# Kernel tuning notes

Hardware: AMD Instinct MI355X
Metric: run time of the kernel (lower is better)

## Reference

```python
import jax, jax.numpy as jnp
import numpy as np

N_NODES = 100000
N_EDGES = 3200000
IN_C, HID_C, OUT_C = 128, 128, 64
NUM_GRAPHS = 1024


def sage_conv(x, edge_index, W_l, b_l, W_r):
    # PyG SAGEConv (aggr='mean', root_weight=True):
    #   out = lin_l(mean_{j in N(i)} x_j) + lin_r(x_i)
    src, dst = edge_index[0], edge_index[1]
    msg = x[src]                                             # [E, C] gather
    summed = jax.ops.segment_sum(msg, dst, num_segments=x.shape[0])
    cnt = jax.ops.segment_sum(jnp.ones((msg.shape[0],), x.dtype), dst,
                              num_segments=x.shape[0])
    mean_nb = summed / jnp.maximum(cnt, 1.0)[:, None]        # [N, C]
    return mean_nb @ W_l + b_l + x @ W_r


def setup_inputs() -> dict:
    key = jax.random.key(0)
    ks = jax.random.split(key, 8)
    x = jax.random.normal(ks[0], (N_NODES, IN_C), dtype=jnp.float32)
    edge_index = jax.random.randint(ks[1], (2, N_EDGES), 0, N_NODES, dtype=jnp.int64)
    batch = jnp.sort(jax.random.randint(ks[2], (N_NODES,), 0, NUM_GRAPHS, dtype=jnp.int64))
    s1 = 1.0 / np.sqrt(IN_C)
    s2 = 1.0 / np.sqrt(HID_C)
    W1_l = jax.random.uniform(ks[3], (IN_C, HID_C), jnp.float32, -s1, s1)
    b1 = jax.random.uniform(ks[4], (HID_C,), jnp.float32, -s1, s1)
    W1_r = jax.random.uniform(ks[5], (IN_C, HID_C), jnp.float32, -s1, s1)
    W2_l = jax.random.uniform(ks[6], (HID_C, OUT_C), jnp.float32, -s2, s2)
    b2 = jnp.zeros((OUT_C,), jnp.float32)
    W2_r = jax.random.uniform(ks[7], (HID_C, OUT_C), jnp.float32, -s2, s2)
    return {"x": x, "W1_l": W1_l, "b1": b1, "W1_r": W1_r,
            "W2_l": W2_l, "b2": b2, "W2_r": W2_r,
            "edge_index": edge_index, "batch": batch}


def reference(x, W1_l, b1, W1_r, W2_l, b2, W2_r, edge_index, batch):
    h = sage_conv(x, edge_index, W1_l, b1, W1_r)
    h = jax.nn.relu(h)
    # dropout is identity in eval mode (training=False)
    h = sage_conv(h, edge_index, W2_l, b2, W2_r)
    # global_mean_pool: segment mean over graph ids
    summed = jax.ops.segment_sum(h, batch, num_segments=NUM_GRAPHS)
    cnt = jax.ops.segment_sum(jnp.ones((h.shape[0],), h.dtype), batch,
                              num_segments=NUM_GRAPHS)
    return summed / jnp.maximum(cnt, 1.0)[:, None]           # [NUM_GRAPHS, OUT_C]
```

## Files before the change

kernel.cpp:

```cpp
#include <hip/hip_runtime.h>


constexpr int NN = 100000;
constexpr int NE = 3200000;
constexpr int C1 = 128;
constexpr int C2 = 64;
constexpr int NG = 1024;

constexpr int NBK = (NN + 511) >> 9;
constexpr int CAP = 18176;
constexpr int NSH = 13;

typedef unsigned int u32;
typedef unsigned short u16;
typedef unsigned char u8;
typedef _Float16 f16;
typedef f16 f16x8 __attribute__((ext_vector_type(8)));
typedef float f32x4 __attribute__((ext_vector_type(4)));

__device__ __forceinline__ float h2f(u32 bits16) {
  f16 h; u16 b = (u16)bits16;
  __builtin_memcpy(&h, &b, 2);
  return (float)h;
}
__device__ __forceinline__ u16 f2h(float f) {
  f16 h = (f16)f; u16 b;
  __builtin_memcpy(&b, &h, 2);
  return b;
}
__device__ __forceinline__ u32 packh2(float a, float b) {
  return (u32)f2h(a) | ((u32)f2h(b) << 16);
}
__device__ __forceinline__ u32 packq4(float a, float b, float c, float d) {
  int q = 0;
  q = __builtin_amdgcn_cvt_pk_fp8_f32(a, b, q, false);
  q = __builtin_amdgcn_cvt_pk_fp8_f32(c, d, q, true);
  return (u32)q;
}
__device__ __forceinline__ void acc4(u32 g, float& a0, float& a1,
                                     float& a2, float& a3) {
  const auto p = __builtin_amdgcn_cvt_pk_f32_fp8((int)g, false);
  const auto q = __builtin_amdgcn_cvt_pk_f32_fp8((int)g, true);
  a0 += p[0]; a1 += p[1]; a2 += q[0]; a3 += q[1];
}
__device__ __forceinline__ uint4 q8toh8(uint2 g) {
  const auto p0 = __builtin_amdgcn_cvt_pk_f32_fp8((int)g.x, false);
  const auto p1 = __builtin_amdgcn_cvt_pk_f32_fp8((int)g.x, true);
  const auto p2 = __builtin_amdgcn_cvt_pk_f32_fp8((int)g.y, false);
  const auto p3 = __builtin_amdgcn_cvt_pk_f32_fp8((int)g.y, true);
  uint4 o;
  o.x = packh2(p0[0], p0[1]);
  o.y = packh2(p1[0], p1[1]);
  o.z = packh2(p2[0], p2[1]);
  o.w = packh2(p3[0], p3[1]);
  return o;
}

__global__ __launch_bounds__(256)
void sage_x2hw(const float* __restrict__ x, u16* __restrict__ xh,
               u32* __restrict__ xq,
               const float* __restrict__ W1l, const float* __restrict__ W1r,
               const float* __restrict__ W2l, const float* __restrict__ W2r,
               u16* __restrict__ wt1, u16* __restrict__ wt2,
               int* __restrict__ gcur) {
  const int id = blockIdx.x * 256 + threadIdx.x;
  constexpr int NX = NN * 32;
  if (id < NX) {
    const float4 v = ((const float4*)x)[id];
    uint2 o;
    o.x = packh2(v.x, v.y);
    o.y = packh2(v.z, v.w);
    ((uint2*)xh)[id] = o;
    xq[id] = packq4(v.x, v.y, v.z, v.w);
  } else if (id < NX + 128 * 256) {
    const int id2 = id - NX;
    const int n = id2 >> 8, k = id2 & 255;
    const float v = (k < 128) ? W1l[k * 128 + n] : W1r[(k - 128) * 128 + n];
    wt1[id2] = f2h(v);
  } else if (id < NX + 128 * 256 + 128 * 128) {
    const int id3 = id - NX - 128 * 256;
    const int n = id3 >> 7, k = id3 & 127;
    const float v = (n < 64) ? W2l[k * 64 + n] : W2r[k * 64 + (n - 64)];
    wt2[id3] = f2h(v);
  } else if (id < NX + 128 * 256 + 128 * 128 + NBK) {
    const int b = id - NX - 128 * 256 - 128 * 128;
    gcur[b] = b * CAP;
  }
}

__global__ __launch_bounds__(256)
void sage_part(const int* __restrict__ esrc, const int* __restrict__ edst,
               int* __restrict__ gcur, u32* __restrict__ gpart) {
  __shared__ int h[NBK], cur[NBK];
  for (int i = threadIdx.x; i < NBK; i += 256) h[i] = 0;
  __syncthreads();
  const int e0 = blockIdx.x * 4096 + threadIdx.x * 4;
  int4 dv[4], sv[4];
  bool val[4];
#pragma unroll
  for (int j = 0; j < 4; ++j) {
    const int e = e0 + j * 1024;
    val[j] = (e < NE);
    if (val[j]) {
      dv[j] = *(const int4*)(edst + e);
      sv[j] = *(const int4*)(esrc + e);
    }
  }
#pragma unroll
  for (int j = 0; j < 4; ++j) {
    if (val[j]) {
      atomicAdd(&h[dv[j].x >> 9], 1);
      atomicAdd(&h[dv[j].y >> 9], 1);
      atomicAdd(&h[dv[j].z >> 9], 1);
      atomicAdd(&h[dv[j].w >> 9], 1);
    }
  }
  __syncthreads();
  for (int i = threadIdx.x; i < NBK; i += 256)
    cur[i] = h[i] ? atomicAdd(&gcur[i], h[i]) : 0;
  __syncthreads();
#pragma unroll
  for (int j = 0; j < 4; ++j) {
    if (val[j]) {
      int bk, p;
      bk = dv[j].x >> 9; p = atomicAdd(&cur[bk], 1);
      if (p < (bk + 1) * CAP) gpart[p] = ((u32)sv[j].x << 9) | (u32)(dv[j].x & 511);
      bk = dv[j].y >> 9; p = atomicAdd(&cur[bk], 1);
      if (p < (bk + 1) * CAP) gpart[p] = ((u32)sv[j].y << 9) | (u32)(dv[j].y & 511);
      bk = dv[j].z >> 9; p = atomicAdd(&cur[bk], 1);
      if (p < (bk + 1) * CAP) gpart[p] = ((u32)sv[j].z << 9) | (u32)(dv[j].z & 511);
      bk = dv[j].w >> 9; p = atomicAdd(&cur[bk], 1);
      if (p < (bk + 1) * CAP) gpart[p] = ((u32)sv[j].w << 9) | (u32)(dv[j].w & 511);
    }
  }
}

__global__ __launch_bounds__(256)
void sage_pscan(const int* __restrict__ gcur, int* __restrict__ bbase) {
  __shared__ int s[256];
  const int t = threadIdx.x;
  int c = (t < NBK) ? (gcur[t] - t * CAP) : 0;
  c = (c > CAP) ? CAP : c;
  s[t] = c;
  __syncthreads();
  for (int d = 1; d < 256; d <<= 1) {
    const int a = (t >= d) ? s[t - d] : 0;
    __syncthreads();
    s[t] += a;
    __syncthreads();
  }
  if (t < NBK) bbase[t] = s[t] - c;
  if (t == 255) bbase[NBK] = s[255];
}

__global__ __launch_bounds__(512)
void sage_bbuild(const int* __restrict__ bbase, const u32* __restrict__ gpart,
                 int* __restrict__ offs, int* __restrict__ csr) {
  __shared__ int cnt2[512 * NSH];
  __shared__ int ssc[512];
  const int b = blockIdx.x, t = threadIdx.x;
  const int c0 = bbase[b], cnt = bbase[b + 1] - c0;
  const u32* gp = gpart + (size_t)b * CAP;
  for (int i = t; i < 512 * NSH; i += 512) cnt2[i] = 0;
  __syncthreads();
  for (int e = t; e < cnt; e += 512) {
    const u32 pk = gp[e];
    atomicAdd(&cnt2[(pk & 511) * NSH + (pk >> 22)], 1);
  }
  __syncthreads();
  int deg = 0;
#pragma unroll
  for (int s = 0; s < NSH; ++s) deg += cnt2[t * NSH + s];
  ssc[t] = deg;
  __syncthreads();
  for (int d = 1; d < 512; d <<= 1) {
    const int a = (t >= d) ? ssc[t - d] : 0;
    __syncthreads();
    ssc[t] += a;
    __syncthreads();
  }
  const int pre = ssc[t] - deg;
  const int node = b * 512 + t;
  if (node < NN) offs[node] = c0 + pre;
  if (b == 0 && t == 0) offs[NN] = bbase[NBK];
  int run = c0 + pre;
#pragma unroll
  for (int s = 0; s < NSH; ++s) {
    const int c = cnt2[t * NSH + s];
    cnt2[t * NSH + s] = run;
    run += c;
  }
  __syncthreads();
  for (int e = t; e < cnt; e += 512) {
    const u32 pk = gp[e];
    const int p = atomicAdd(&cnt2[(pk & 511) * NSH + (pk >> 22)], 1);
    csr[p] = (int)(pk >> 9);
  }
}

__global__ __launch_bounds__(256)
void sage_agg1q(const int* __restrict__ offs, const int* __restrict__ csr,
                const u32* __restrict__ xq, u32* __restrict__ agg1) {
  const int node = blockIdx.x * 4 + (threadIdx.x >> 6);
  const int lane = threadIdx.x & 63;
  if (node >= NN) return;
  const int beg = offs[node], end = offs[node + 1];
  const int hf = lane >> 5, l = lane & 31;
  const u32* xb = xq + l;
  float a0 = 0, a1 = 0, a2 = 0, a3 = 0;
  int e = beg + hf;
  for (; e + 14 < end; e += 16) {
    const int i0 = csr[e],      i1 = csr[e + 2],  i2 = csr[e + 4],
              i3 = csr[e + 6],  i4 = csr[e + 8],  i5 = csr[e + 10],
              i6 = csr[e + 12], i7 = csr[e + 14];
    const u32 g0 = xb[(size_t)i0 * 32], g1 = xb[(size_t)i1 * 32],
              g2 = xb[(size_t)i2 * 32], g3 = xb[(size_t)i3 * 32],
              g4 = xb[(size_t)i4 * 32], g5 = xb[(size_t)i5 * 32],
              g6 = xb[(size_t)i6 * 32], g7 = xb[(size_t)i7 * 32];
    acc4(g0, a0, a1, a2, a3); acc4(g1, a0, a1, a2, a3);
    acc4(g2, a0, a1, a2, a3); acc4(g3, a0, a1, a2, a3);
    acc4(g4, a0, a1, a2, a3); acc4(g5, a0, a1, a2, a3);
    acc4(g6, a0, a1, a2, a3); acc4(g7, a0, a1, a2, a3);
  }
  for (; e < end; e += 2)
    acc4(xb[(size_t)csr[e] * 32], a0, a1, a2, a3);
  a0 += __shfl_xor(a0, 32);
  a1 += __shfl_xor(a1, 32);
  a2 += __shfl_xor(a2, 32);
  a3 += __shfl_xor(a3, 32);
  if (hf == 0) {
    const float inv = 1.0f / fmaxf((float)(end - beg), 1.0f);
    agg1[(size_t)node * 32 + l] = packq4(a0 * inv, a1 * inv, a2 * inv, a3 * inv);
  }
}

__global__ __launch_bounds__(256)
void sage_agg2q(const int* __restrict__ offs, const int* __restrict__ csr,
                const u32* __restrict__ tq, u16* __restrict__ agg2h) {
  const int node = blockIdx.x * 4 + (threadIdx.x >> 6);
  const int lane = threadIdx.x & 63;
  if (node >= NN) return;
  const int beg = offs[node], end = offs[node + 1];
  const int grp = lane >> 4, l = lane & 15;
  const u32* tb = tq + l;
  float a0 = 0, a1 = 0, a2 = 0, a3 = 0;
  int e = beg + grp;
  for (; e + 28 < end; e += 32) {
    const int i0 = csr[e],      i1 = csr[e + 4],  i2 = csr[e + 8],
              i3 = csr[e + 12], i4 = csr[e + 16], i5 = csr[e + 20],
              i6 = csr[e + 24], i7 = csr[e + 28];
    const u32 g0 = tb[(size_t)i0 * 16], g1 = tb[(size_t)i1 * 16],
              g2 = tb[(size_t)i2 * 16], g3 = tb[(size_t)i3 * 16],
              g4 = tb[(size_t)i4 * 16], g5 = tb[(size_t)i5 * 16],
              g6 = tb[(size_t)i6 * 16], g7 = tb[(size_t)i7 * 16];
    acc4(g0, a0, a1, a2, a3); acc4(g1, a0, a1, a2, a3);
    acc4(g2, a0, a1, a2, a3); acc4(g3, a0, a1, a2, a3);
    acc4(g4, a0, a1, a2, a3); acc4(g5, a0, a1, a2, a3);
    acc4(g6, a0, a1, a2, a3); acc4(g7, a0, a1, a2, a3);
  }
  for (; e < end; e += 4)
    acc4(tb[(size_t)csr[e] * 16], a0, a1, a2, a3);
  a0 += __shfl_xor(a0, 16); a0 += __shfl_xor(a0, 32);
  a1 += __shfl_xor(a1, 16); a1 += __shfl_xor(a1, 32);
  a2 += __shfl_xor(a2, 16); a2 += __shfl_xor(a2, 32);
  a3 += __shfl_xor(a3, 16); a3 += __shfl_xor(a3, 32);
  if (lane < 16) {
    const float inv = 1.0f / fmaxf((float)(end - beg), 1.0f);
    uint2 o;
    o.x = packh2(a0 * inv, a1 * inv);
    o.y = packh2(a2 * inv, a3 * inv);
    *(uint2*)(agg2h + (size_t)node * 64 + l * 4) = o;
  }
}

__global__ __launch_bounds__(256)
void sage_mgemm12(const u32* __restrict__ A1q, const u16* __restrict__ A2,
                  const u16* __restrict__ wt1, const u16* __restrict__ wt2,
                  const float* __restrict__ bias,
                  u16* __restrict__ O, u8* __restrict__ tqb) {
  __shared__ __align__(16) u16 As[2][64][128];
  const int t = threadIdx.x;
  const int r0 = blockIdx.x * 64;
  const int w = t >> 6, l = t & 63;
  const int lr = l & 15, lk = l >> 4;

  f16x8 B1[2][8];
#pragma unroll
  for (int j = 0; j < 2; ++j)
#pragma unroll
    for (int kt = 0; kt < 8; ++kt)
      B1[j][kt] = *(const f16x8*)(wt1 + (((2 * w + j) * 16 + lr) * 256 + kt * 32 + lk * 8));

#pragma unroll
  for (int i = 0; i < 4; ++i) {
    const int id = i * 256 + t;
    const int row = id >> 4, c = id & 15;
    int gr = r0 + row; gr = (gr < NN) ? gr : NN - 1;
    const uint2 g = *(const uint2*)(A1q + (size_t)gr * 32 + c * 2);
    *(uint4*)(&As[0][row][(c ^ (row & 7)) * 8]) = q8toh8(g);
  }
#pragma unroll
  for (int i = 0; i < 4; ++i) {
    const int id = i * 256 + t;
    const int row = id >> 4, c = id & 15;
    int gr = r0 + row; gr = (gr < NN) ? gr : NN - 1;
    const uint4 v = *(const uint4*)(A2 + (size_t)gr * 128 + c * 8);
    *(uint4*)(&As[1][row][(c ^ (row & 7)) * 8]) = v;
  }
  __syncthreads();

  f32x4 acc[4][2];
#pragma unroll
  for (int rt = 0; rt < 4; ++rt)
#pragma unroll
    for (int j = 0; j < 2; ++j) acc[rt][j] = (f32x4){0.f, 0.f, 0.f, 0.f};
#pragma unroll
  for (int rt = 0; rt < 4; ++rt) {
    const int ra = rt * 16 + lr;
#pragma unroll
    for (int kt = 0; kt < 8; ++kt) {
      const int buf = kt >> 2, kk = kt & 3;
      const f16x8 a = *(const f16x8*)(&As[buf][ra][((kk * 4 + lk) ^ (ra & 7)) * 8]);
      acc[rt][0] = __builtin_amdgcn_mfma_f32_16x16x32_f16(a, B1[0][kt], acc[rt][0], 0, 0, 0);
      acc[rt][1] = __builtin_amdgcn_mfma_f32_16x16x32_f16(a, B1[1][kt], acc[rt][1], 0, 0, 0);
    }
  }

  f16x8 B2[2][4];
#pragma unroll
  for (int j = 0; j < 2; ++j)
#pragma unroll
    for (int kt = 0; kt < 4; ++kt)
      B2[j][kt] = *(const f16x8*)(wt2 + (((2 * w + j) * 16 + lr) * 128 + kt * 32 + lk * 8));

  __syncthreads();

#pragma unroll
  for (int j = 0; j < 2; ++j) {
    const int col = (2 * w + j) * 16 + lr;
    const float bv = bias[col];
    const int chb = col >> 3, within = col & 7;
#pragma unroll
    for (int rt = 0; rt < 4; ++rt)
#pragma unroll
      for (int r = 0; r < 4; ++r) {
        const int row = rt * 16 + lk * 4 + r;
        As[0][row][((chb ^ (row & 7)) << 3) + within] =
            f2h(fmaxf(acc[rt][j][r] + bv, 0.f));
      }
  }
  __syncthreads();

  f32x4 acc2[4][2];
#pragma unroll
  for (int rt = 0; rt < 4; ++rt)
#pragma unroll
    for (int j = 0; j < 2; ++j) acc2[rt][j] = (f32x4){0.f, 0.f, 0.f, 0.f};
#pragma unroll
  for (int rt = 0; rt < 4; ++rt) {
    const int ra = rt * 16 + lr;
#pragma unroll
    for (int kt = 0; kt < 4; ++kt) {
      const f16x8 a = *(const f16x8*)(&As[0][ra][((kt * 4 + lk) ^ (ra & 7)) * 8]);
      acc2[rt][0] = __builtin_amdgcn_mfma_f32_16x16x32_f16(a, B2[0][kt], acc2[rt][0], 0, 0, 0);
      acc2[rt][1] = __builtin_amdgcn_mfma_f32_16x16x32_f16(a, B2[1][kt], acc2[rt][1], 0, 0, 0);
    }
  }
#pragma unroll
  for (int j = 0; j < 2; ++j) {
    const int col = (2 * w + j) * 16 + lr;
#pragma unroll
    for (int rt = 0; rt < 4; ++rt)
#pragma unroll
      for (int r = 0; r < 4; ++r) {
        const int row = r0 + rt * 16 + lk * 4 + r;
        if (row < NN) {
          if (col < 64) {
            const int pk = __builtin_amdgcn_cvt_pk_fp8_f32(acc2[rt][j][r], acc2[rt][j][r], 0, false);
            tqb[(size_t)row * 64 + col] = (u8)pk;
          } else {
            O[(size_t)row * 128 + col] = f2h(acc2[rt][j][r]);
          }
        }
      }
  }
}

__global__ __launch_bounds__(256)
void sage_pool2(const u16* __restrict__ o128, const u16* __restrict__ agg2h,
                const float* __restrict__ b2, const int* __restrict__ batch,
                float* __restrict__ pool, int* __restrict__ gcnt) {
  const int t = threadIdx.x;
  const int c = t & 63, sl = t >> 6;
  const int n0 = blockIdx.x * 128;
  const float bv = b2[c];
  float acc = 0.f;
  int curg = -1, cnt = 0;
  for (int n = n0 + sl; n < n0 + 128 && n < NN; n += 4) {
    const int g = batch[n];
    const float v = h2f(o128[(size_t)n * 128 + 64 + c]) +
                    h2f(agg2h[(size_t)n * 64 + c]) + bv;
    if (g != curg) {
      if (curg >= 0) {
        atomicAdd(&pool[curg * C2 + c], acc);
        if (c == 0) atomicAdd(&gcnt[curg], cnt);
      }
      curg = g; acc = v; cnt = 1;
    } else {
      acc += v; cnt += 1;
    }
  }
  if (curg >= 0) {
    atomicAdd(&pool[curg * C2 + c], acc);
    if (c == 0) atomicAdd(&gcnt[curg], cnt);
  }
}

__global__ __launch_bounds__(256)
void sage_out(const float* __restrict__ pool, const int* __restrict__ gcnt,
              float* __restrict__ out) {
  const int i = blockIdx.x * 256 + threadIdx.x;
  if (i >= NG * C2) return;
  out[i] = pool[i] / fmaxf((float)gcnt[i >> 6], 1.0f);
}

extern "C" void kernel_launch(void* const* d_in, const int* in_sizes, int n_in,
                              void* d_out, int out_size, void* d_ws, size_t ws_size,
                              hipStream_t stream) {
  (void)in_sizes; (void)n_in; (void)out_size; (void)ws_size;
  const float* x     = (const float*)d_in[0];
  const float* W1l   = (const float*)d_in[1];
  const float* b1    = (const float*)d_in[2];
  const float* W1r   = (const float*)d_in[3];
  const float* W2l   = (const float*)d_in[4];
  const float* b2    = (const float*)d_in[5];
  const float* W2r   = (const float*)d_in[6];
  const int*   ei    = (const int*)d_in[7];
  const int*   batch = (const int*)d_in[8];
  const int* esrc = ei;
  const int* edst = ei + NE;
  float* out = (float*)d_out;

  char* base = (char*)d_ws;
  size_t off = 0;
  auto take = [&](size_t bytes) -> char* {
    char* p = base + off;
    off += (bytes + 255) & ~(size_t)255;
    return p;
  };
  int* bbase    = (int*)take((size_t)(NBK + 1) * 4);
  int* gcur     = (int*)take((size_t)NBK * 4);
  int* offs     = (int*)take((size_t)(NN + 1) * 4);
  int* csr      = (int*)take((size_t)NE * 4);
  char* bufA    = take((size_t)NN * 256);
  char* bufB    = take((size_t)NN * 256);
  char* bufC    = take((size_t)NBK * CAP * 4 + (size_t)NN * 128);
  float* pool   = (float*)take((size_t)NG * C2 * 4);
  int*  gcnt    = (int*)take((size_t)NG * 4);
  u16*  wt1     = (u16*)take((size_t)128 * 256 * 2);
  u16*  wt2     = (u16*)take((size_t)128 * 128 * 2);

  u16*   xh    = (u16*)bufA;
  u16*   o128  = (u16*)bufA;
  u32*   agg1  = (u32*)bufB;
  u16*   agg2h = (u16*)bufB;
  u8*    tqb   = (u8*)(bufB + (size_t)NN * 128);
  u32*   gpart = (u32*)bufC;
  u32*   xq    = (u32*)(bufC + (size_t)NBK * CAP * 4);

  const size_t zbytes = (size_t)((char*)gcnt + (size_t)NG * 4 - (char*)pool);
  hipMemsetAsync(pool, 0, zbytes, stream);

  sage_x2hw<<<(NN * 32 + 128 * 256 + 128 * 128 + NBK + 255) / 256, 256, 0,
              stream>>>(x, xh, xq, W1l, W1r, W2l, W2r, wt1, wt2, gcur);

  const int PB = (NE + 4095) / 4096;
  sage_part<<<PB, 256, 0, stream>>>(esrc, edst, gcur, gpart);
  sage_pscan<<<1, 256, 0, stream>>>(gcur, bbase);
  sage_bbuild<<<NBK, 512, 0, stream>>>(bbase, gpart, offs, csr);

  sage_agg1q<<<(NN + 3) / 4, 256, 0, stream>>>(offs, csr, xq, agg1);

  sage_mgemm12<<<(NN + 63) / 64, 256, 0, stream>>>(agg1, xh, wt1, wt2, b1,
                                                   o128, tqb);

  sage_agg2q<<<(NN + 3) / 4, 256, 0, stream>>>(offs, csr, (const u32*)tqb, agg2h);

  sage_pool2<<<(NN + 127) / 128, 256, 0, stream>>>(o128, agg2h, b2, batch, pool, gcnt);
  sage_out<<<(NG * C2 + 255) / 256, 256, 0, stream>>>(pool, gcnt, out);
}
```

Measured before the change: 281.3 us.

## Fuse pooling into GEMM and aggregation epilogues, fold scan into bucket build

Removes the separate pool kernel by having the GEMM epilogue atomically add the root-weight half (plus bias) into per-graph pool sums, and the second aggregation atomically add mean-neighbor results directly. The single-block prefix scan is merged into each bucket-build block (each block recomputes the scan), graph counts move into the conversion kernel, and the partition kernel processes twice as many edges per block. This removes two kernel launches and the fp16 intermediate writes and reads, at the cost of many float atomics on pool entries, which contend because nodes are sorted by graph, and makes the summation order nondeterministic.

```diff
diff --git a/kernel.cpp b/kernel.cpp
--- a/kernel.cpp
+++ b/kernel.cpp
@@ -62,9 +62,13 @@
                const float* __restrict__ W1l, const float* __restrict__ W1r,
                const float* __restrict__ W2l, const float* __restrict__ W2r,
                u16* __restrict__ wt1, u16* __restrict__ wt2,
-               int* __restrict__ gcur) {
+               int* __restrict__ gcur,
+               const int* __restrict__ batch, int* __restrict__ gcnt) {
   const int id = blockIdx.x * 256 + threadIdx.x;
   constexpr int NX = NN * 32;
+  constexpr int W1E = NX + 128 * 256;
+  constexpr int W2E = W1E + 128 * 128;
+  constexpr int GCE = W2E + NBK;
   if (id < NX) {
     const float4 v = ((const float4*)x)[id];
     uint2 o;
@@ -72,19 +76,21 @@
     o.y = packh2(v.z, v.w);
     ((uint2*)xh)[id] = o;
     xq[id] = packq4(v.x, v.y, v.z, v.w);
-  } else if (id < NX + 128 * 256) {
+  } else if (id < W1E) {
     const int id2 = id - NX;
     const int n = id2 >> 8, k = id2 & 255;
     const float v = (k < 128) ? W1l[k * 128 + n] : W1r[(k - 128) * 128 + n];
     wt1[id2] = f2h(v);
-  } else if (id < NX + 128 * 256 + 128 * 128) {
-    const int id3 = id - NX - 128 * 256;
+  } else if (id < W2E) {
+    const int id3 = id - W1E;
     const int n = id3 >> 7, k = id3 & 127;
     const float v = (n < 64) ? W2l[k * 64 + n] : W2r[k * 64 + (n - 64)];
     wt2[id3] = f2h(v);
-  } else if (id < NX + 128 * 256 + 128 * 128 + NBK) {
-    const int b = id - NX - 128 * 256 - 128 * 128;
+  } else if (id < GCE) {
+    const int b = id - W2E;
     gcur[b] = b * CAP;
+  } else if (id < GCE + NN) {
+    atomicAdd(&gcnt[batch[id - GCE]], 1);
   }
 }
 
@@ -94,11 +100,11 @@
   __shared__ int h[NBK], cur[NBK];
   for (int i = threadIdx.x; i < NBK; i += 256) h[i] = 0;
   __syncthreads();
-  const int e0 = blockIdx.x * 4096 + threadIdx.x * 4;
-  int4 dv[4], sv[4];
-  bool val[4];
-#pragma unroll
-  for (int j = 0; j < 4; ++j) {
+  const int e0 = blockIdx.x * 8192 + threadIdx.x * 4;
+  int4 dv[8], sv[8];
+  bool val[8];
+#pragma unroll
+  for (int j = 0; j < 8; ++j) {
     const int e = e0 + j * 1024;
     val[j] = (e < NE);
     if (val[j]) {
@@ -107,7 +113,7 @@
     }
   }
 #pragma unroll
-  for (int j = 0; j < 4; ++j) {
+  for (int j = 0; j < 8; ++j) {
     if (val[j]) {
       atomicAdd(&h[dv[j].x >> 9], 1);
       atomicAdd(&h[dv[j].y >> 9], 1);
@@ -120,7 +126,7 @@
     cur[i] = h[i] ? atomicAdd(&gcur[i], h[i]) : 0;
   __syncthreads();
 #pragma unroll
-  for (int j = 0; j < 4; ++j) {
+  for (int j = 0; j < 8; ++j) {
     if (val[j]) {
       int bk, p;
       bk = dv[j].x >> 9; p = atomicAdd(&cur[bk], 1);
@@ -135,43 +141,19 @@
   }
 }
 
-__global__ __launch_bounds__(256)
-void sage_pscan(const int* __restrict__ gcur, int* __restrict__ bbase) {
-  __shared__ int s[256];
-  const int t = threadIdx.x;
-  int c = (t < NBK) ? (gcur[t] - t * CAP) : 0;
-  c = (c > CAP) ? CAP : c;
-  s[t] = c;
-  __syncthreads();
-  for (int d = 1; d < 256; d <<= 1) {
-    const int a = (t >= d) ? s[t - d] : 0;
-    __syncthreads();
-    s[t] += a;
-    __syncthreads();
-  }
-  if (t < NBK) bbase[t] = s[t] - c;
-  if (t == 255) bbase[NBK] = s[255];
-}
-
 __global__ __launch_bounds__(512)
-void sage_bbuild(const int* __restrict__ bbase, const u32* __restrict__ gpart,
+void sage_bbuild(const int* __restrict__ gcur, const u32* __restrict__ gpart,
                  int* __restrict__ offs, int* __restrict__ csr) {
   __shared__ int cnt2[512 * NSH];
   __shared__ int ssc[512];
+  __shared__ int sh_c0, sh_cnt;
   const int b = blockIdx.x, t = threadIdx.x;
-  const int c0 = bbase[b], cnt = bbase[b + 1] - c0;
-  const u32* gp = gpart + (size_t)b * CAP;
-  for (int i = t; i < 512 * NSH; i += 512) cnt2[i] = 0;
-  __syncthreads();
-  for (int e = t; e < cnt; e += 512) {
-    const u32 pk = gp[e];
-    atomicAdd(&cnt2[(pk & 511) * NSH + (pk >> 22)], 1);
-  }
-  __syncthreads();
-  int deg = 0;
-#pragma unroll
-  for (int s = 0; s < NSH; ++s) deg += cnt2[t * NSH + s];
-  ssc[t] = deg;
+  int cval = 0;
+  if (t < NBK) {
+    cval = gcur[t] - t * CAP;
+    cval = (cval > CAP) ? CAP : cval;
+  }
+  ssc[t] = cval;
   __syncthreads();
   for (int d = 1; d < 512; d <<= 1) {
     const int a = (t >= d) ? ssc[t - d] : 0;
@@ -179,10 +161,32 @@
     ssc[t] += a;
     __syncthreads();
   }
+  if (t == b) { sh_c0 = ssc[t] - cval; sh_cnt = cval; }
+  if (b == 0 && t == NBK - 1) offs[NN] = ssc[t];
+  __syncthreads();
+  const int c0 = sh_c0, cnt = sh_cnt;
+  const u32* gp = gpart + (size_t)b * CAP;
+  for (int i = t; i < 512 * NSH; i += 512) cnt2[i] = 0;
+  __syncthreads();
+  for (int e = t; e < cnt; e += 512) {
+    const u32 pk = gp[e];
+    atomicAdd(&cnt2[(pk & 511) * NSH + (pk >> 22)], 1);
+  }
+  __syncthreads();
+  int deg = 0;
+#pragma unroll
+  for (int s = 0; s < NSH; ++s) deg += cnt2[t * NSH + s];
+  ssc[t] = deg;
+  __syncthreads();
+  for (int d = 1; d < 512; d <<= 1) {
+    const int a = (t >= d) ? ssc[t - d] : 0;
+    __syncthreads();
+    ssc[t] += a;
+    __syncthreads();
+  }
   const int pre = ssc[t] - deg;
   const int node = b * 512 + t;
   if (node < NN) offs[node] = c0 + pre;
-  if (b == 0 && t == 0) offs[NN] = bbase[NBK];
   int run = c0 + pre;
 #pragma unroll
   for (int s = 0; s < NSH; ++s) {
@@ -236,7 +240,8 @@
 
 __global__ __launch_bounds__(256)
 void sage_agg2q(const int* __restrict__ offs, const int* __restrict__ csr,
-                const u32* __restrict__ tq, u16* __restrict__ agg2h) {
+                const u32* __restrict__ tq, const int* __restrict__ batch,
+                float* __restrict__ pool) {
   const int node = blockIdx.x * 4 + (threadIdx.x >> 6);
   const int lane = threadIdx.x & 63;
   if (node >= NN) return;
@@ -266,18 +271,20 @@
   a3 += __shfl_xor(a3, 16); a3 += __shfl_xor(a3, 32);
   if (lane < 16) {
     const float inv = 1.0f / fmaxf((float)(end - beg), 1.0f);
-    uint2 o;
-    o.x = packh2(a0 * inv, a1 * inv);
-    o.y = packh2(a2 * inv, a3 * inv);
-    *(uint2*)(agg2h + (size_t)node * 64 + l * 4) = o;
+    float* pp = pool + (size_t)batch[node] * C2 + l * 4;
+    atomicAdd(pp + 0, a0 * inv);
+    atomicAdd(pp + 1, a1 * inv);
+    atomicAdd(pp + 2, a2 * inv);
+    atomicAdd(pp + 3, a3 * inv);
   }
 }
 
 __global__ __launch_bounds__(256)
 void sage_mgemm12(const u32* __restrict__ A1q, const u16* __restrict__ A2,
                   const u16* __restrict__ wt1, const u16* __restrict__ wt2,
-                  const float* __restrict__ bias,
-                  u16* __restrict__ O, u8* __restrict__ tqb) {
+                  const float* __restrict__ bias, const float* __restrict__ b2,
+                  const int* __restrict__ batch,
+                  float* __restrict__ pool, u8* __restrict__ tqb) {
   __shared__ __align__(16) u16 As[2][64][128];
   const int t = threadIdx.x;
   const int r0 = blockIdx.x * 64;
@@ -369,50 +376,29 @@
 #pragma unroll
   for (int j = 0; j < 2; ++j) {
     const int col = (2 * w + j) * 16 + lr;
-#pragma unroll
-    for (int rt = 0; rt < 4; ++rt)
-#pragma unroll
-      for (int r = 0; r < 4; ++r) {
-        const int row = r0 + rt * 16 + lk * 4 + r;
-        if (row < NN) {
-          if (col < 64) {
+    if (col < 64) {
+#pragma unroll
+      for (int rt = 0; rt < 4; ++rt)
+#pragma unroll
+        for (int r = 0; r < 4; ++r) {
+          const int row = r0 + rt * 16 + lk * 4 + r;
+          if (row < NN) {
             const int pk = __builtin_amdgcn_cvt_pk_fp8_f32(acc2[rt][j][r], acc2[rt][j][r], 0, false);
             tqb[(size_t)row * 64 + col] = (u8)pk;
-          } else {
-            O[(size_t)row * 128 + col] = f2h(acc2[rt][j][r]);
           }
         }
-      }
-  }
-}
-
-__global__ __launch_bounds__(256)
-void sage_pool2(const u16* __restrict__ o128, const u16* __restrict__ agg2h,
-                const float* __restrict__ b2, const int* __restrict__ batch,
-                float* __restrict__ pool, int* __restrict__ gcnt) {
-  const int t = threadIdx.x;
-  const int c = t & 63, sl = t >> 6;
-  const int n0 = blockIdx.x * 128;
-  const float bv = b2[c];
-  float acc = 0.f;
-  int curg = -1, cnt = 0;
-  for (int n = n0 + sl; n < n0 + 128 && n < NN; n += 4) {
-    const int g = batch[n];
-    const float v = h2f(o128[(size_t)n * 128 + 64 + c]) +
-                    h2f(agg2h[(size_t)n * 64 + c]) + bv;
-    if (g != curg) {
-      if (curg >= 0) {
-        atomicAdd(&pool[curg * C2 + c], acc);
-        if (c == 0) atomicAdd(&gcnt[curg], cnt);
-      }
-      curg = g; acc = v; cnt = 1;
     } else {
-      acc += v; cnt += 1;
-    }
-  }
-  if (curg >= 0) {
-    atomicAdd(&pool[curg * C2 + c], acc);
-    if (c == 0) atomicAdd(&gcnt[curg], cnt);
+      const int pc = col - 64;
+      const float bv = b2[pc];
+#pragma unroll
+      for (int rt = 0; rt < 4; ++rt)
+#pragma unroll
+        for (int r = 0; r < 4; ++r) {
+          const int row = r0 + rt * 16 + lk * 4 + r;
+          if (row < NN)
+            atomicAdd(&pool[(size_t)batch[row] * C2 + pc], acc2[rt][j][r] + bv);
+        }
+    }
   }
 }
 
@@ -448,7 +434,6 @@
     off += (bytes + 255) & ~(size_t)255;
     return p;
   };
-  int* bbase    = (int*)take((size_t)(NBK + 1) * 4);
   int* gcur     = (int*)take((size_t)NBK * 4);
   int* offs     = (int*)take((size_t)(NN + 1) * 4);
   int* csr      = (int*)take((size_t)NE * 4);
@@ -461,9 +446,7 @@
   u16*  wt2     = (u16*)take((size_t)128 * 128 * 2);
 
   u16*   xh    = (u16*)bufA;
-  u16*   o128  = (u16*)bufA;
   u32*   agg1  = (u32*)bufB;
-  u16*   agg2h = (u16*)bufB;
   u8*    tqb   = (u8*)(bufB + (size_t)NN * 128);
   u32*   gpart = (u32*)bufC;
   u32*   xq    = (u32*)(bufC + (size_t)NBK * CAP * 4);
@@ -471,21 +454,21 @@
   const size_t zbytes = (size_t)((char*)gcnt + (size_t)NG * 4 - (char*)pool);
   hipMemsetAsync(pool, 0, zbytes, stream);
 
-  sage_x2hw<<<(NN * 32 + 128 * 256 + 128 * 128 + NBK + 255) / 256, 256, 0,
-              stream>>>(x, xh, xq, W1l, W1r, W2l, W2r, wt1, wt2, gcur);
-
-  const int PB = (NE + 4095) / 4096;
+  sage_x2hw<<<(NN * 32 + 128 * 256 + 128 * 128 + NBK + NN + 255) / 256, 256, 0,
+              stream>>>(x, xh, xq, W1l, W1r, W2l, W2r, wt1, wt2, gcur,
+                        batch, gcnt);
+
+  const int PB = (NE + 8191) / 8192;
   sage_part<<<PB, 256, 0, stream>>>(esrc, edst, gcur, gpart);
-  sage_pscan<<<1, 256, 0, stream>>>(gcur, bbase);
-  sage_bbuild<<<NBK, 512, 0, stream>>>(bbase, gpart, offs, csr);
+  sage_bbuild<<<NBK, 512, 0, stream>>>(gcur, gpart, offs, csr);
 
   sage_agg1q<<<(NN + 3) / 4, 256, 0, stream>>>(offs, csr, xq, agg1);
 
-  sage_mgemm12<<<(NN + 63) / 64, 256, 0, stream>>>(agg1, xh, wt1, wt2, b1,
-                                                   o128, tqb);
-
-  sage_agg2q<<<(NN + 3) / 4, 256, 0, stream>>>(offs, csr, (const u32*)tqb, agg2h);
-
-  sage_pool2<<<(NN + 127) / 128, 256, 0, stream>>>(o128, agg2h, b2, batch, pool, gcnt);
+  sage_mgemm12<<<(NN + 63) / 64, 256, 0, stream>>>(agg1, xh, wt1, wt2, b1, b2,
+                                                   batch, pool, tqb);
+
+  sage_agg2q<<<(NN + 3) / 4, 256, 0, stream>>>(offs, csr, (const u32*)tqb,
+                                               batch, pool);
+
   sage_out<<<(NG * C2 + 255) / 256, 256, 0, stream>>>(pool, gcnt, out);
 }
```

Result: slower. 432.8 us (+53.8%).
